# Kernel tuning notes

Measured on AMD Instinct MI355X. Metric: run time of the kernel, lower is better.

Reference implementation:

```python
import jax, jax.numpy as jnp
import numpy as np

EPS = 1e-6
BN_EPS = 1e-5  # torch BatchNorm default eps
B, H, L, D = 4, 8, 128, 64


def _bn(x, gamma, beta, axes):
    # training-mode batchnorm: biased batch stats over `axes`, per-channel (dim 1) affine
    mu = jnp.mean(x, axis=axes, keepdims=True)
    var = jnp.var(x, axis=axes, keepdims=True)
    shape = [1] * x.ndim
    shape[1] = -1
    return (x - mu) * jax.lax.rsqrt(var + BN_EPS) * gamma.reshape(shape) + beta.reshape(shape)


def setup_inputs() -> dict:
    key = jax.random.key(0)
    kq, kk, kv = jax.random.split(key, 3)
    return {
        "Q": jax.random.normal(kq, (B, H, L, D), jnp.float32),
        "K": jax.random.normal(kk, (B, H, L, D), jnp.float32),
        "V": jax.random.uniform(kv, (B, H, L, D), jnp.float32),
        "j_gamma": jnp.ones((H,), jnp.float32),
        "j_beta": jnp.zeros((H,), jnp.float32),
        "h_gamma": jnp.ones((H,), jnp.float32),
        "h_beta": jnp.zeros((H,), jnp.float32),
        "bnH_gamma": jnp.ones((H,), jnp.float32),
        "bnH_beta": jnp.zeros((H,), jnp.float32),
    }


def reference(Q, K, V, j_gamma, j_beta, h_gamma, h_beta, bnH_gamma, bnH_beta):
    # normalize V into a distribution over D, entropy terms
    Vn = V / (jnp.sum(V, axis=-1, keepdims=True) + EPS)
    Vn = jnp.clip(Vn, EPS, 1.0)
    hi = -Vn * jnp.log2(Vn)            # [B,H,L,D]
    h = jnp.sum(hi, axis=-1)           # [B,H,L]

    pQ = jax.nn.softmax(Q, axis=-1)
    pK = jax.nn.softmax(K, axis=-1)
    pQe = pQ[:, :, :, None, :]         # [B,H,L,1,D]
    pKe = pK[:, :, None, :, :]         # [B,H,1,L,D]
    m = 0.5 * (pQe + pKe)              # [B,H,L,L,D] -- dominant intermediate
    kl_q = jnp.sum(pQe * jnp.log2(pQe / (m + EPS) + EPS), axis=-1)  # [B,H,L,L]
    kl_k = jnp.sum(pKe * jnp.log2(pKe / (m + EPS) + EPS), axis=-1)
    J = 0.5 * kl_q + 0.5 * kl_k        # [B,H,L,L]

    # batchnorm only the off-diagonal entries of J (channel = head)
    rows, cols = np.nonzero(~np.eye(L, dtype=bool))
    nd = J[:, :, rows, cols]           # [B,H,L*(L-1)]
    nd = _bn(nd, j_gamma, j_beta, (0, 2))
    J = J.at[:, :, rows, cols].set(nd)

    h = _bn(h, h_gamma, h_beta, (0, 2))

    # QUBO solver stand-in (original detaches + CPU round-trip): binary x per node,
    # greedy heuristic for min x^T J x + h^T x, treated as a constant.
    x = jax.lax.stop_gradient((jnp.sum(J, axis=-1) + h < 0).astype(J.dtype))  # [B,H,L]

    # per-node energy contribution H_i = x_i * ((J x)_i + h_i)
    He = x * (jnp.einsum('bhij,bhj->bhi', J, x) + h)  # [B,H,L]

    Hd = He[..., None] * hi / h[..., None]            # [B,H,L,D]
    Hd = _bn(-Hd, bnH_gamma, bnH_beta, (0, 2, 3))
    return Hd
```

## Files before the change

kernel.cpp:

```cpp
#include <hip/hip_runtime.h>


#define EPS 1e-6f
#define BN_EPS 1e-5f

__global__ void __launch_bounds__(64) k0_rows(
    const float* __restrict__ K, const float* __restrict__ V,
    float* __restrict__ pK, float* __restrict__ Sk,
    float* __restrict__ hi, float* __restrict__ h_raw)
{
    const int r = blockIdx.x;
    const int lane = threadIdx.x;
    const int base = r * 64 + lane;

    float kk = K[base];
    float m = kk;
    for (int off = 32; off; off >>= 1) m = fmaxf(m, __shfl_xor(m, off));
    float e = __expf(kk - m);
    float s = e;
    for (int off = 32; off; off >>= 1) s += __shfl_xor(s, off);
    const float pk = e * __fdividef(1.0f, s);
    pK[base] = pk;
    float pl = pk * __log2f(pk);
    for (int off = 32; off; off >>= 1) pl += __shfl_xor(pl, off);
    if (lane == 0) Sk[r] = pl;

    float v = V[base];
    s = v;
    for (int off = 32; off; off >>= 1) s += __shfl_xor(s, off);
    float vn = v * __fdividef(1.0f, s + EPS);
    vn = fminf(fmaxf(vn, EPS), 1.0f);
    const float hv = -vn * __log2f(vn);
    hi[base] = hv;
    float hs = hv;
    for (int off = 32; off; off >>= 1) hs += __shfl_xor(hs, off);
    if (lane == 0) h_raw[r] = hs;
}

__global__ void __launch_bounds__(256) ka_J(
    const float* __restrict__ Q, const float* __restrict__ pK,
    const float* __restrict__ Sk,
    float* __restrict__ J, float* __restrict__ Sg, float* __restrict__ Dg,
    double* __restrict__ Jpart)
{
    __shared__ float sK[128 * 65];
    __shared__ float sQ[4 * 64];
    __shared__ float sSk[128];
    __shared__ double sred[8];
    const int bid = blockIdx.x;
    const int n = bid >> 5;
    const int i0 = (bid & 31) * 4;
    const int tid = threadIdx.x;
    const int wave = tid >> 6, lane = tid & 63;
    const int gi = i0 + wave;
    const int R = n * 128 + gi;

    float q = Q[R * 64 + lane];
    float mq = q;
    for (int off = 32; off; off >>= 1) mq = fmaxf(mq, __shfl_xor(mq, off));
    float eq = __expf(q - mq);
    float sq = eq;
    for (int off = 32; off; off >>= 1) sq += __shfl_xor(sq, off);
    const float pq = eq * __fdividef(1.0f, sq);
    sQ[wave * 64 + lane] = pq;
    float bq = pq * __log2f(pq);
    for (int off = 32; off; off >>= 1) bq += __shfl_xor(bq, off);

    const float4* pk4 = (const float4*)(pK + n * 8192);
    #pragma unroll
    for (int v = 0; v < 8; ++v) {
        const int idx = tid + 256 * v;
        const float4 f = pk4[idx];
        float* dst = sK + (idx >> 4) * 65 + (idx & 15) * 4;
        dst[0] = f.x; dst[1] = f.y; dst[2] = f.z; dst[3] = f.w;
    }
    if (tid < 128) sSk[tid] = Sk[n * 128 + tid];
    __syncthreads();

    const float* qrow = sQ + wave * 64;
    const float* kp0 = sK + lane * 65;
    const float* kp1 = sK + (lane + 64) * 65;
    float a0 = 0.f, a1 = 0.f;
    #pragma unroll 8
    for (int d = 0; d < 64; ++d) {
        const float qv = qrow[d];
        const float s0v = qv + kp0[d];
        const float s1v = qv + kp1[d];
        a0 += s0v * __log2f(fmaf(0.5f, s0v, EPS));
        a1 += s1v * __log2f(fmaf(0.5f, s1v, EPS));
    }
    const float J0 = 0.5f * (bq + sSk[lane]      - a0);
    const float J1 = 0.5f * (bq + sSk[lane + 64] - a1);
    const int rbase = R * 128;
    J[rbase + lane] = J0;
    J[rbase + lane + 64] = J1;

    float s0 = J0 + J1;
    for (int off = 32; off; off >>= 1) s0 += __shfl_xor(s0, off);
    const float D = (gi < 64) ? __shfl(J0, gi) : __shfl(J1, gi - 64);
    if (lane == 0) { Sg[R] = s0; Dg[R] = D; }

    double ls = 0.0, ls2 = 0.0;
    if (lane != gi)      { ls += J0; ls2 += (double)J0 * (double)J0; }
    if (lane + 64 != gi) { ls += J1; ls2 += (double)J1 * (double)J1; }
    for (int off = 32; off; off >>= 1) {
        ls  += __shfl_xor(ls, off);
        ls2 += __shfl_xor(ls2, off);
    }
    if (lane == 0) { sred[wave] = ls; sred[4 + wave] = ls2; }
    __syncthreads();
    if (tid == 0) {
        Jpart[2 * bid]     = sred[0] + sred[1] + sred[2] + sred[3];
        Jpart[2 * bid + 1] = sred[4] + sred[5] + sred[6] + sred[7];
    }
}

__global__ void __launch_bounds__(256) kc_he(
    const float* __restrict__ J, const float* __restrict__ hi,
    const double* __restrict__ Jpart, const float* __restrict__ h_raw,
    const float* __restrict__ Sg, const float* __restrict__ Dg,
    const float* __restrict__ j_gamma, const float* __restrict__ j_beta,
    const float* __restrict__ h_gamma, const float* __restrict__ h_beta,
    float* __restrict__ t, double* __restrict__ tblk)
{
    __shared__ float sx[128], shbn[128];
    __shared__ double sred[8];
    __shared__ double st1[4], st2[4];
    __shared__ float sprm[5];
    const int bid = blockIdx.x;
    const int n = bid >> 4;
    const int i0 = (bid & 15) * 8;
    const int hh = n & 7;
    const int tid = threadIdx.x;
    const int wave = tid >> 6, lane = tid & 63;

    if (wave == 0) {
        const int p1 = lane, p2 = lane + 64;
        const int pb1 = ((p1 >> 5) * 8 + hh) * 32 + (p1 & 31);
        const int pb2 = ((p2 >> 5) * 8 + hh) * 32 + (p2 & 31);
        double s = Jpart[2 * pb1] + Jpart[2 * pb2];
        double s2 = Jpart[2 * pb1 + 1] + Jpart[2 * pb2 + 1];
        for (int off = 32; off; off >>= 1) {
            s += __shfl_xor(s, off); s2 += __shfl_xor(s2, off);
        }
        if (lane == 0) {
            const double cnt = 65024.0;
            const double mean = s / cnt;
            const double var = s2 / cnt - mean * mean;
            sprm[0] = (float)mean;
            sprm[1] = (float)(1.0 / sqrt(var + (double)BN_EPS));
        }
    }
    {
        double s = 0.0, s2 = 0.0;
        for (int p = tid; p < 512; p += 256) {
            const int b = p >> 7, l = p & 127;
            const float v = h_raw[(b * 8 + hh) * 128 + l];
            s += v; s2 += (double)v * (double)v;
        }
        for (int off = 32; off; off >>= 1) {
            s += __shfl_xor(s, off); s2 += __shfl_xor(s2, off);
        }
        if (lane == 0) { sred[wave] = s; sred[4 + wave] = s2; }
    }
    __syncthreads();
    if (tid == 0) {
        const double hs = sred[0] + sred[1] + sred[2] + sred[3];
        const double hs2 = sred[4] + sred[5] + sred[6] + sred[7];
        const double hm = hs / 512.0;
        const double hvar = hs2 / 512.0 - hm * hm;
        sprm[2] = (float)hm;
        sprm[3] = (float)(1.0 / sqrt(hvar + (double)BN_EPS));
    }
    __syncthreads();
    const float jm = sprm[0], jinv = sprm[1];
    const float hm = sprm[2], hinv = sprm[3];
    const float jg = j_gamma[hh], jb = j_beta[hh];
    if (tid < 128) {
        const int i = tid;
        const float S = Sg[n * 128 + i], D = Dg[n * 128 + i];
        const float hb = (h_raw[n * 128 + i] - hm) * hinv * h_gamma[hh] + h_beta[hh];
        const float rs = jinv * jg * (S - D - 127.0f * jm) + 127.0f * jb + D;
        sx[i] = (rs + hb < 0.0f) ? 1.0f : 0.0f;
        shbn[i] = hb;
    }
    __syncthreads();
    if (wave == 0) {
        float c = sx[lane] + sx[lane + 64];
        for (int off = 32; off; off >>= 1) c += __shfl_xor(c, off);
        if (lane == 0) sprm[4] = c;
    }
    __syncthreads();
    const float C = sprm[4];
    const int rb = wave;
    double bs = 0.0, bs2 = 0.0;
    for (int rr = 0; rr < 2; ++rr) {
        const int i = i0 + rb + 4 * rr;
        const int r = n * 128 + i;
        float tr = J[r * 128 + lane] * sx[lane] + J[r * 128 + 64 + lane] * sx[lane + 64];
        for (int off = 32; off; off >>= 1) tr += __shfl_xor(tr, off);
        const float xi = sx[i], Di = Dg[r];
        const float dot = jinv * jg * (tr - xi * Di - jm * (C - xi))
                        + jb * (C - xi) + xi * Di;
        const float He = xi * (dot + shbn[i]);
        const float tv = -(He * hi[r * 64 + lane] * __fdividef(1.0f, shbn[i]));
        t[r * 64 + lane] = tv;
        double ds = tv, ds2 = (double)tv * (double)tv;
        for (int off = 32; off; off >>= 1) {
            ds += __shfl_xor(ds, off); ds2 += __shfl_xor(ds2, off);
        }
        if (lane == 0) { bs += ds; bs2 += ds2; }
    }
    if (lane == 0) { st1[wave] = bs; st2[wave] = bs2; }
    __syncthreads();
    if (tid == 0) {
        tblk[2 * bid]     = st1[0] + st1[1] + st1[2] + st1[3];
        tblk[2 * bid + 1] = st2[0] + st2[1] + st2[2] + st2[3];
    }
}

__global__ void __launch_bounds__(256) kd_out(
    const double* __restrict__ tblk, const float* __restrict__ t,
    const float* __restrict__ gamma, const float* __restrict__ beta,
    float* __restrict__ out)
{
    __shared__ double sm[2];
    const int bid = blockIdx.x;
    const int tid = threadIdx.x;
    const int g0 = bid * 512;
    const int hh = (g0 >> 13) & 7;
    if (tid < 64) {
        const int b = tid >> 4, tile = tid & 15;
        const int cb = ((b * 8 + hh) << 4) + tile;
        double s = tblk[2 * cb], s2 = tblk[2 * cb + 1];
        for (int off = 32; off; off >>= 1) {
            s += __shfl_xor(s, off); s2 += __shfl_xor(s2, off);
        }
        if (tid == 0) { sm[0] = s; sm[1] = s2; }
    }
    __syncthreads();
    const double mean = sm[0] / 32768.0;
    const double var = sm[1] / 32768.0 - mean * mean;
    const float tm = (float)mean;
    const float tinv = (float)(1.0 / sqrt(var + (double)BN_EPS));
    const float g = gamma[hh], be = beta[hh];
    out[g0 + tid]       = (t[g0 + tid]       - tm) * tinv * g + be;
    out[g0 + 256 + tid] = (t[g0 + 256 + tid] - tm) * tinv * g + be;
}

extern "C" void kernel_launch(void* const* d_in, const int* in_sizes, int n_in,
                              void* d_out, int out_size, void* d_ws, size_t ws_size,
                              hipStream_t stream) {
    (void)in_sizes; (void)n_in; (void)out_size; (void)ws_size;
    const float* Q = (const float*)d_in[0];
    const float* K = (const float*)d_in[1];
    const float* V = (const float*)d_in[2];
    const float* j_gamma = (const float*)d_in[3];
    const float* j_beta  = (const float*)d_in[4];
    const float* h_gamma = (const float*)d_in[5];
    const float* h_beta  = (const float*)d_in[6];
    const float* bnH_gamma = (const float*)d_in[7];
    const float* bnH_beta  = (const float*)d_in[8];
    float* out = (float*)d_out;

    float* w = (float*)d_ws;
    float*  J     = w;
    float*  hi    = w + 524288;
    float*  t     = w + 786432;
    float*  pK    = w + 1310720;
    float*  h_raw = w + 1572864;
    float*  Sk    = w + 1581056;
    float*  Sg    = w + 1585152;
    float*  Dg    = w + 1589248;
    double* Jpart = (double*)(w + 1593344);
    double* tblk  = (double*)(w + 1597440);

    k0_rows<<<4096, 64, 0, stream>>>(K, V, pK, Sk, hi, h_raw);
    ka_J<<<1024, 256, 0, stream>>>(Q, pK, Sk, J, Sg, Dg, Jpart);
    kc_he<<<512, 256, 0, stream>>>(J, hi, Jpart, h_raw, Sg, Dg,
                                   j_gamma, j_beta, h_gamma, h_beta, t, tblk);
    kd_out<<<512, 256, 0, stream>>>(tblk, t, bnH_gamma, bnH_beta, out);
}
```

Measured before the change: 92.68 us.

## Fuse K-softmax and V-entropy row prep into the J kernel

Removes the separate per-row kernel that computed softmax(K), its entropy term, and the V-entropy terms. The J kernel now loads raw K into shared memory and computes softmax plus the sum of p*log2(p) for all 128 K rows in every block. Each block also computes hi and h_raw for its own 4 rows of V. This saves one launch and the pK/Sk round trip through global memory, at the cost of every block recomputing softmax for the whole K slab, which is 32x redundant work per batch-head.

```diff
diff --git a/kernel.cpp b/kernel.cpp
--- a/kernel.cpp
+++ b/kernel.cpp
@@ -4,44 +4,12 @@
 #define EPS 1e-6f
 #define BN_EPS 1e-5f
 
-__global__ void __launch_bounds__(64) k0_rows(
-    const float* __restrict__ K, const float* __restrict__ V,
-    float* __restrict__ pK, float* __restrict__ Sk,
+__global__ void __launch_bounds__(256) kab_J(
+    const float* __restrict__ Q, const float* __restrict__ K,
+    const float* __restrict__ V,
+    float* __restrict__ J, float* __restrict__ Sg, float* __restrict__ Dg,
+    double* __restrict__ Jpart,
     float* __restrict__ hi, float* __restrict__ h_raw)
-{
-    const int r = blockIdx.x;
-    const int lane = threadIdx.x;
-    const int base = r * 64 + lane;
-
-    float kk = K[base];
-    float m = kk;
-    for (int off = 32; off; off >>= 1) m = fmaxf(m, __shfl_xor(m, off));
-    float e = __expf(kk - m);
-    float s = e;
-    for (int off = 32; off; off >>= 1) s += __shfl_xor(s, off);
-    const float pk = e * __fdividef(1.0f, s);
-    pK[base] = pk;
-    float pl = pk * __log2f(pk);
-    for (int off = 32; off; off >>= 1) pl += __shfl_xor(pl, off);
-    if (lane == 0) Sk[r] = pl;
-
-    float v = V[base];
-    s = v;
-    for (int off = 32; off; off >>= 1) s += __shfl_xor(s, off);
-    float vn = v * __fdividef(1.0f, s + EPS);
-    vn = fminf(fmaxf(vn, EPS), 1.0f);
-    const float hv = -vn * __log2f(vn);
-    hi[base] = hv;
-    float hs = hv;
-    for (int off = 32; off; off >>= 1) hs += __shfl_xor(hs, off);
-    if (lane == 0) h_raw[r] = hs;
-}
-
-__global__ void __launch_bounds__(256) ka_J(
-    const float* __restrict__ Q, const float* __restrict__ pK,
-    const float* __restrict__ Sk,
-    float* __restrict__ J, float* __restrict__ Sg, float* __restrict__ Dg,
-    double* __restrict__ Jpart)
 {
     __shared__ float sK[128 * 65];
     __shared__ float sQ[4 * 64];
@@ -55,6 +23,15 @@
     const int gi = i0 + wave;
     const int R = n * 128 + gi;
 
+    const float4* k4 = (const float4*)(K + n * 8192);
+    #pragma unroll
+    for (int v = 0; v < 8; ++v) {
+        const int idx = tid + 256 * v;
+        const float4 f = k4[idx];
+        float* dst = sK + (idx >> 4) * 65 + (idx & 15) * 4;
+        dst[0] = f.x; dst[1] = f.y; dst[2] = f.z; dst[3] = f.w;
+    }
+
     float q = Q[R * 64 + lane];
     float mq = q;
     for (int off = 32; off; off >>= 1) mq = fmaxf(mq, __shfl_xor(mq, off));
@@ -66,15 +43,34 @@
     float bq = pq * __log2f(pq);
     for (int off = 32; off; off >>= 1) bq += __shfl_xor(bq, off);
 
-    const float4* pk4 = (const float4*)(pK + n * 8192);
-    #pragma unroll
-    for (int v = 0; v < 8; ++v) {
-        const int idx = tid + 256 * v;
-        const float4 f = pk4[idx];
-        float* dst = sK + (idx >> 4) * 65 + (idx & 15) * 4;
-        dst[0] = f.x; dst[1] = f.y; dst[2] = f.z; dst[3] = f.w;
-    }
-    if (tid < 128) sSk[tid] = Sk[n * 128 + tid];
+    {
+        float v = V[R * 64 + lane];
+        float s = v;
+        for (int off = 32; off; off >>= 1) s += __shfl_xor(s, off);
+        float vn = v * __fdividef(1.0f, s + EPS);
+        vn = fminf(fmaxf(vn, EPS), 1.0f);
+        const float hv = -vn * __log2f(vn);
+        hi[R * 64 + lane] = hv;
+        float hs = hv;
+        for (int off = 32; off; off >>= 1) hs += __shfl_xor(hs, off);
+        if (lane == 0) h_raw[R] = hs;
+    }
+    __syncthreads();
+
+    for (int rr = 0; rr < 32; ++rr) {
+        const int r = wave * 32 + rr;
+        float kk = sK[r * 65 + lane];
+        float m = kk;
+        for (int off = 32; off; off >>= 1) m = fmaxf(m, __shfl_xor(m, off));
+        float e = __expf(kk - m);
+        float s = e;
+        for (int off = 32; off; off >>= 1) s += __shfl_xor(s, off);
+        const float pk = e * __fdividef(1.0f, s);
+        sK[r * 65 + lane] = pk;
+        float pl = pk * __log2f(pk);
+        for (int off = 32; off; off >>= 1) pl += __shfl_xor(pl, off);
+        if (lane == 0) sSk[r] = pl;
+    }
     __syncthreads();
 
     const float* qrow = sQ + wave * 64;
@@ -267,16 +263,13 @@
     float*  J     = w;
     float*  hi    = w + 524288;
     float*  t     = w + 786432;
-    float*  pK    = w + 1310720;
     float*  h_raw = w + 1572864;
-    float*  Sk    = w + 1581056;
     float*  Sg    = w + 1585152;
     float*  Dg    = w + 1589248;
     double* Jpart = (double*)(w + 1593344);
     double* tblk  = (double*)(w + 1597440);
 
-    k0_rows<<<4096, 64, 0, stream>>>(K, V, pK, Sk, hi, h_raw);
-    ka_J<<<1024, 256, 0, stream>>>(Q, pK, Sk, J, Sg, Dg, Jpart);
+    kab_J<<<1024, 256, 0, stream>>>(Q, K, V, J, Sg, Dg, Jpart, hi, h_raw);
     kc_he<<<512, 256, 0, stream>>>(J, hi, Jpart, h_raw, Sg, Dg,
                                    j_gamma, j_beta, h_gamma, h_beta, t, tblk);
     kd_out<<<512, 256, 0, stream>>>(tblk, t, bnH_gamma, bnH_beta, out);
```

Measured after the change: 115.1 us. +24.2%, slower.
